# Optimization experiments

Measured on AMD Instinct MI355X. Metric: run time of the kernel, lower is better.

## Reference

```python
import jax, jax.numpy as jnp
import numpy as np

K_BITS = 4
V_BITS = 4
GROUP_SIZE = 64
EPS = 1e-8


def _quant_dequant_per_token(x, bits):
    # TurboQuantProd: symmetric per-token (per head_dim vector) absmax quantization.
    qmax = 2.0 ** (bits - 1) - 1.0
    scale = jnp.maximum(jnp.max(jnp.abs(x), axis=-1, keepdims=True) / qmax, EPS)
    return jnp.clip(jnp.round(x / scale), -qmax, qmax) * scale


def _quant_dequant_grouped(x, bits, group_size):
    # TurboQuantValue: symmetric grouped absmax quantization along head_dim.
    shp = x.shape
    xg = x.reshape(shp[:-1] + (shp[-1] // group_size, group_size))
    qmax = 2.0 ** (bits - 1) - 1.0
    scale = jnp.maximum(jnp.max(jnp.abs(xg), axis=-1, keepdims=True) / qmax, EPS)
    dq = jnp.clip(jnp.round(xg / scale), -qmax, qmax) * scale
    return dq.reshape(shp)


def setup_inputs() -> dict:
    key = jax.random.key(0)
    kq, kk, kv = jax.random.split(key, 3)
    B, H, S, D = 2, 16, 2048, 128
    query = jax.random.normal(kq, (B, H, S, D), dtype=jnp.float32)
    k = jax.random.normal(kk, (B, H, S, D), dtype=jnp.float32)
    v = jax.random.normal(kv, (B, H, S, D), dtype=jnp.float32)
    causal_mask = jnp.tril(jnp.ones((S, S), dtype=bool))[None, None]  # [1,1,S,S]
    return {"query": query, "key": k, "value": v, "causal_mask": causal_mask}


def reference(query, key, value, causal_mask):
    # Non-protected path: quantize K per-token, V grouped, then fused dequant + SDPA.
    head_dim = query.shape[-1]
    scale = 1.0 / np.sqrt(head_dim).astype(np.float32)
    dq_key = _quant_dequant_per_token(key, K_BITS)
    dq_value = _quant_dequant_grouped(value, V_BITS, GROUP_SIZE)
    scores = jnp.einsum('bhqd,bhkd->bhqk', query, dq_key) * scale
    scores = jnp.where(causal_mask, scores, -jnp.inf)
    weights = jax.nn.softmax(scores, axis=-1)
    output = jnp.einsum('bhqk,bhkd->bhqd', weights, dq_value)
    return (output, weights)
```

## Files before the change

kernel.cpp:

```cpp
#include <hip/hip_runtime.h>

#define SQ 2048
#define DD 128
#define BHN 32
#define SC2 0.12751741934f

typedef __attribute__((ext_vector_type(8))) short bf16x8;
typedef __attribute__((ext_vector_type(4))) float f32x4;

__device__ __forceinline__ unsigned short f2bf(float x){
  unsigned int u = __float_as_uint(x);
  unsigned int r = (u + 0x7FFFu + ((u >> 16) & 1u)) >> 16;
  return (unsigned short)r;
}
__device__ __forceinline__ unsigned pack2bf(float a, float b){
  return (unsigned)f2bf(a) | ((unsigned)f2bf(b) << 16);
}

__device__ __forceinline__ void gl_lds16(const void* g, void* l){
  __builtin_amdgcn_global_load_lds(
      (const __attribute__((address_space(1))) unsigned int*)g,
      (__attribute__((address_space(3))) unsigned int*)l, 16, 0, 0);
}

__global__ __launch_bounds__(256) void qd_kernel(const float* __restrict__ K,
                                                 const float* __restrict__ V,
                                                 char* __restrict__ dqK,
                                                 char* __restrict__ dqVt){
  __shared__ float Vlds[128*65];
  const int t = threadIdx.x;
  const int bh = blockIdx.x >> 5;
  const int stile = blockIdx.x & 31;
  const int tt = t >> 2;
  const int q4 = t & 3;
  const int s = stile*64 + tt;
  const long ebase = ((long)(bh*SQ + s))*DD + 32*q4;

  float vals[32];
  {
    const float4* kp = (const float4*)(K + ebase);
    float am = 0.f;
    #pragma unroll
    for (int j=0;j<8;j++){
      float4 v4 = kp[j];
      vals[4*j+0]=v4.x; vals[4*j+1]=v4.y; vals[4*j+2]=v4.z; vals[4*j+3]=v4.w;
      am = fmaxf(am, fmaxf(fmaxf(fabsf(v4.x),fabsf(v4.y)),fmaxf(fabsf(v4.z),fabsf(v4.w))));
    }
    am = fmaxf(am, __shfl_xor(am,1));
    am = fmaxf(am, __shfl_xor(am,2));
    const float sc = fmaxf(am/7.0f, 1e-8f);
    #pragma unroll
    for (int j=0;j<32;j++){
      float qv = rintf(vals[j]/sc);
      qv = fminf(7.f, fmaxf(-7.f, qv));
      vals[j] = qv*sc;
    }
    const long rowb = ((long)(bh*SQ + s))*256;
    const int swz = (s & 7) << 4;
    #pragma unroll
    for (int c=0;c<4;c++){
      uint4 w;
      w.x = pack2bf(vals[8*c+0], vals[8*c+1]);
      w.y = pack2bf(vals[8*c+2], vals[8*c+3]);
      w.z = pack2bf(vals[8*c+4], vals[8*c+5]);
      w.w = pack2bf(vals[8*c+6], vals[8*c+7]);
      *(uint4*)(dqK + rowb + ((64*q4 + 16*c) ^ swz)) = w;
    }
  }
  {
    const float4* vp = (const float4*)(V + ebase);
    float am = 0.f;
    #pragma unroll
    for (int j=0;j<8;j++){
      float4 v4 = vp[j];
      vals[4*j+0]=v4.x; vals[4*j+1]=v4.y; vals[4*j+2]=v4.z; vals[4*j+3]=v4.w;
      am = fmaxf(am, fmaxf(fmaxf(fabsf(v4.x),fabsf(v4.y)),fmaxf(fabsf(v4.z),fabsf(v4.w))));
    }
    am = fmaxf(am, __shfl_xor(am,1));
    const float sc = fmaxf(am/7.0f, 1e-8f);
    #pragma unroll
    for (int j=0;j<32;j++){
      float qv = rintf(vals[j]/sc);
      qv = fminf(7.f, fmaxf(-7.f, qv));
      Vlds[(32*q4 + j)*65 + tt] = qv*sc;
    }
  }
  __syncthreads();
  #pragma unroll
  for (int m=0;m<4;m++){
    const int chunk = m*256 + t;
    const int d = chunk >> 3;
    const int c = chunk & 7;
    uint4 w;
    const float* f = &Vlds[d*65 + 8*c];
    w.x = pack2bf(f[0], f[1]);
    w.y = pack2bf(f[2], f[3]);
    w.z = pack2bf(f[4], f[5]);
    w.w = pack2bf(f[6], f[7]);
    const long ob = ((long)(bh*DD + d))*4096 + (long)stile*128 + ((16*c) ^ ((d&7)<<4));
    *(uint4*)(dqVt + ob) = w;
  }
}

__global__ __launch_bounds__(512,2) void attn1_kernel(const float* __restrict__ Q,
    const char* __restrict__ dqK, const char* __restrict__ dqVt,
    float* __restrict__ Out, float* __restrict__ SinvG){
  __shared__ __attribute__((aligned(16))) char Kt[2][16384];
  __shared__ __attribute__((aligned(16))) char Vt[2][16384];
  __shared__ __attribute__((aligned(16))) char Et[8][4096];

  const int bid = blockIdx.x;
  const int xcd = bid & 7;
  const int loc = bid >> 3;
  const int bh  = xcd*4 + (loc & 3);
  const int p   = loc >> 2;
  const int t = threadIdx.x;
  const int lane = t & 63;
  const int w = t >> 6;
  const int s = w >> 2;
  const int ws = w & 3;
  const int l15 = lane & 15, l4 = lane >> 4;
  const int swz = (l15 & 7) << 4;

  const int qt   = s ? p : (15 - p);
  const int q0   = qt * 128;
  const int nktA = 2*(15 - p) + 2;
  const int nktB = 2*p + 2;
  const int myNkt = s ? nktB : nktA;
  const int rbase = q0 + 32*ws;

  bf16x8 qa[2][4];
  #pragma unroll
  for (int g=0; g<2; ++g){
    const float* qb = Q + ((long)(bh*SQ) + rbase + 16*g + l15)*DD + 8*l4;
    #pragma unroll
    for (int kk=0;kk<4;kk++){
      float4 a = *(const float4*)(qb + 32*kk);
      float4 b = *(const float4*)(qb + 32*kk + 4);
      bf16x8 r;
      r[0]=(short)f2bf(a.x); r[1]=(short)f2bf(a.y); r[2]=(short)f2bf(a.z); r[3]=(short)f2bf(a.w);
      r[4]=(short)f2bf(b.x); r[5]=(short)f2bf(b.y); r[6]=(short)f2bf(b.z); r[7]=(short)f2bf(b.w);
      qa[g][kk]=r;
    }
  }

  const char* Kb = dqK + (long)bh*SQ*256;
  const char* Vb = dqVt + (long)bh*DD*4096;

  const f32x4 z4 = {0.f,0.f,0.f,0.f};
  f32x4 oacc[2][8] = {{z4,z4,z4,z4,z4,z4,z4,z4},{z4,z4,z4,z4,z4,z4,z4,z4}};
  float ssum[2] = {0.f, 0.f};
  char* eb = &Et[w][0];

  auto stage = [&](int buf, int kt){
    const char* ks = Kb + (long)kt*16384;
    gl_lds16(ks + t*16,        &Kt[buf][t*16]);
    gl_lds16(ks + 8192 + t*16, &Kt[buf][8192 + t*16]);
    const char* vs = Vb + (long)kt*128;
    gl_lds16(vs + (long)(t>>3)*4096      + (t&7)*16, &Vt[buf][t*16]);
    gl_lds16(vs + (long)(64+(t>>3))*4096 + (t&7)*16, &Vt[buf][8192 + t*16]);
  };

  stage(0, 0);
  __syncthreads();
  int cur = 0;
  for (int kt=0; kt<nktA; ++kt){
    if (kt+1 < nktA) stage(cur^1, kt+1);

    if (kt < myNkt){
      f32x4 sacc[2][4] = {{z4,z4,z4,z4},{z4,z4,z4,z4}};
      {
        const char* kbase = &Kt[cur][0] + l15*256;
        __builtin_amdgcn_s_setprio(1);
        #pragma unroll
        for (int cf=0;cf<4;cf++){
          #pragma unroll
          for (int kk=0;kk<4;kk++){
            bf16x8 kb = *(const bf16x8*)(kbase + cf*4096 + ((64*kk+16*l4) ^ swz));
            sacc[0][cf] = __builtin_amdgcn_mfma_f32_16x16x32_bf16(kb, qa[0][kk], sacc[0][cf], 0,0,0);
            sacc[1][cf] = __builtin_amdgcn_mfma_f32_16x16x32_bf16(kb, qa[1][kk], sacc[1][cf], 0,0,0);
          }
        }
        __builtin_amdgcn_s_setprio(0);
      }

      const int k0 = kt*64;
      if (kt < 2*qt){
        #pragma unroll
        for (int g=0; g<2; ++g){
          const int lr = 16*g + l15;
          #pragma unroll
          for (int cf=0;cf<4;cf++){
            float e0 = exp2f(sacc[g][cf][0]*SC2);
            float e1 = exp2f(sacc[g][cf][1]*SC2);
            float e2 = exp2f(sacc[g][cf][2]*SC2);
            float e3 = exp2f(sacc[g][cf][3]*SC2);
            ssum[g] += (e0+e1) + (e2+e3);
            uint2 wp; wp.x = pack2bf(e0,e1); wp.y = pack2bf(e2,e3);
            *(uint2*)(eb + lr*128 + ((32*cf + 8*l4) ^ swz)) = wp;
          }
        }
      } else {
        #pragma unroll
        for (int g=0; g<2; ++g){
          const int lr = 16*g + l15;
          const int qrow = rbase + lr;
          #pragma unroll
          for (int cf=0;cf<4;cf++){
            const int tok0 = k0 + 16*cf + 4*l4;
            float e0 = (tok0+0 <= qrow) ? exp2f(sacc[g][cf][0]*SC2) : 0.f;
            float e1 = (tok0+1 <= qrow) ? exp2f(sacc[g][cf][1]*SC2) : 0.f;
            float e2 = (tok0+2 <= qrow) ? exp2f(sacc[g][cf][2]*SC2) : 0.f;
            float e3 = (tok0+3 <= qrow) ? exp2f(sacc[g][cf][3]*SC2) : 0.f;
            ssum[g] += (e0+e1) + (e2+e3);
            uint2 wp; wp.x = pack2bf(e0,e1); wp.y = pack2bf(e2,e3);
            *(uint2*)(eb + lr*128 + ((32*cf + 8*l4) ^ swz)) = wp;
          }
        }
      }

      {
        const char* vbase = &Vt[cur][0] + l15*128;
        __builtin_amdgcn_s_setprio(1);
        #pragma unroll
        for (int kc=0;kc<2;kc++){
          const int eo = (64*kc + 16*l4) ^ swz;
          bf16x8 ea0 = *(const bf16x8*)(eb + l15*128 + eo);
          bf16x8 ea1 = *(const bf16x8*)(eb + (16+l15)*128 + eo);
          #pragma unroll
          for (int df=0;df<8;df++){
            bf16x8 vv = *(const bf16x8*)(vbase + df*2048 + eo);
            oacc[0][df] = __builtin_amdgcn_mfma_f32_16x16x32_bf16(ea0, vv, oacc[0][df], 0,0,0);
            oacc[1][df] = __builtin_amdgcn_mfma_f32_16x16x32_bf16(ea1, vv, oacc[1][df], 0,0,0);
          }
        }
        __builtin_amdgcn_s_setprio(0);
      }
    }
    __syncthreads();
    cur ^= 1;
  }

  #pragma unroll
  for (int g=0; g<2; ++g){
    float sm = ssum[g];
    sm += __shfl_xor(sm, 16);
    sm += __shfl_xor(sm, 32);
    const float sinv = 1.0f / sm;
    if (l4 == 0) SinvG[(long)bh*SQ + rbase + 16*g + l15] = sinv;
    float invr[4];
    #pragma unroll
    for (int i=0;i<4;i++) invr[i] = __shfl(sinv, 4*l4+i);
    float* ob = Out + ((long)(bh*SQ) + rbase + 16*g)*DD;
    #pragma unroll
    for (int df=0;df<8;df++){
      #pragma unroll
      for (int i=0;i<4;i++)
        ob[(4*l4+i)*DD + 16*df + l15] = oacc[g][df][i]*invr[i];
    }
  }
}

__global__ __launch_bounds__(256) void attn2_kernel(const float* __restrict__ Q,
    const char* __restrict__ dqK, const float* __restrict__ SinvG,
    float* __restrict__ Wout){
  __shared__ __attribute__((aligned(16))) char Kt[2][16384];

  const int bid = blockIdx.x;
  const int xcd = bid & 7;
  const int loc = bid >> 3;
  const int bh  = xcd*4 + (loc >> 5);
  const int qt  = loc & 31;
  const int q0  = qt * 64;
  const int t = threadIdx.x;
  const int lane = t & 63;
  const int w = t >> 6;
  const int l15 = lane & 15, l4 = lane >> 4;
  const int swz = (l15 & 7) << 4;
  const int qrow = q0 + 16*w + l15;

  bf16x8 qa[4];
  {
    const float* qb = Q + ((long)(bh*SQ) + qrow)*DD + 8*l4;
    #pragma unroll
    for (int kk=0;kk<4;kk++){
      float4 a = *(const float4*)(qb + 32*kk);
      float4 b = *(const float4*)(qb + 32*kk + 4);
      bf16x8 r;
      r[0]=(short)f2bf(a.x); r[1]=(short)f2bf(a.y); r[2]=(short)f2bf(a.z); r[3]=(short)f2bf(a.w);
      r[4]=(short)f2bf(b.x); r[5]=(short)f2bf(b.y); r[6]=(short)f2bf(b.z); r[7]=(short)f2bf(b.w);
      qa[kk]=r;
    }
  }
  const float si = SinvG[(long)bh*SQ + qrow];
  const char* Kb = dqK + (long)bh*SQ*256;
  const int nkt = qt + 1;
  float* Wbase = Wout + (long)bh*SQ*SQ;
  float* wrow  = Wbase + (long)qrow*SQ;

  auto stage = [&](int buf, int kt){
    const char* ks = Kb + (long)kt*16384;
    #pragma unroll
    for (int i=0;i<4;i++)
      gl_lds16(ks + i*4096 + t*16, &Kt[buf][i*4096 + t*16]);
  };

  stage(0,0);
  __syncthreads();
  int cur = 0;
  const f32x4 z4 = {0.f,0.f,0.f,0.f};
  for (int kt=0; kt<nkt; ++kt){
    if (kt+1 < nkt) stage(cur^1, kt+1);
    const int k0 = kt*64;

    f32x4 sacc[4] = {z4,z4,z4,z4};
    {
      const char* kbase = &Kt[cur][0] + l15*256;
      __builtin_amdgcn_s_setprio(1);
      #pragma unroll
      for (int cf=0;cf<4;cf++){
        #pragma unroll
        for (int kk=0;kk<4;kk++){
          bf16x8 kb = *(const bf16x8*)(kbase + cf*4096 + ((64*kk+16*l4) ^ swz));
          sacc[cf] = __builtin_amdgcn_mfma_f32_16x16x32_bf16(kb, qa[kk], sacc[cf], 0,0,0);
        }
      }
      __builtin_amdgcn_s_setprio(0);
    }

    if (kt < qt){
      #pragma unroll
      for (int cf=0;cf<4;cf++){
        const int tok0 = k0 + 16*cf + 4*l4;
        float4 wv;
        wv.x = exp2f(sacc[cf][0]*SC2)*si;
        wv.y = exp2f(sacc[cf][1]*SC2)*si;
        wv.z = exp2f(sacc[cf][2]*SC2)*si;
        wv.w = exp2f(sacc[cf][3]*SC2)*si;
        *(float4*)(wrow + tok0) = wv;
      }
    } else {
      #pragma unroll
      for (int cf=0;cf<4;cf++){
        const int tok0 = k0 + 16*cf + 4*l4;
        float4 wv;
        wv.x = (tok0+0 <= qrow) ? exp2f(sacc[cf][0]*SC2)*si : 0.f;
        wv.y = (tok0+1 <= qrow) ? exp2f(sacc[cf][1]*SC2)*si : 0.f;
        wv.z = (tok0+2 <= qrow) ? exp2f(sacc[cf][2]*SC2)*si : 0.f;
        wv.w = (tok0+3 <= qrow) ? exp2f(sacc[cf][3]*SC2)*si : 0.f;
        *(float4*)(wrow + tok0) = wv;
      }
    }
    __syncthreads();
    cur ^= 1;
  }

  const int z0 = nkt*64;
  if (z0 < SQ){
    float* wr = Wbase + (long)(q0 + 16*w)*SQ;
    const float4 zz = {0.f,0.f,0.f,0.f};
    for (int r=0;r<16;r++){
      float* row = wr + (long)r*SQ;
      for (int c = z0 + 4*lane; c < SQ; c += 256)
        *(float4*)(row + c) = zz;
    }
  }
}

extern "C" void kernel_launch(void* const* d_in, const int* in_sizes, int n_in,
                              void* d_out, int out_size, void* d_ws, size_t ws_size,
                              hipStream_t stream) {
  const float* Q = (const float*)d_in[0];
  const float* K = (const float*)d_in[1];
  const float* V = (const float*)d_in[2];
  float* Out = (float*)d_out;
  float* Wout = (float*)d_out + (size_t)BHN*SQ*DD;
  char* dqK  = (char*)d_ws;
  char* dqVt = (char*)d_ws + (size_t)BHN*SQ*DD*2;
  float* SinvG = (float*)((char*)d_ws + (size_t)BHN*SQ*DD*4);

  qd_kernel<<<BHN*32, 256, 0, stream>>>(K, V, dqK, dqVt);
  attn1_kernel<<<256, 512, 0, stream>>>(Q, dqK, dqVt, Out, SinvG);
  attn2_kernel<<<1024, 256, 0, stream>>>(Q, dqK, SinvG, Wout);
}
```

Before: 280.9 us.

## Split attn1 into smaller 256-thread blocks and reorder attn2 block scheduling

attn1 now uses 256-thread blocks, each handling two 64-row query tiles paired as (31-p, p) for causal load balance, instead of 512-thread blocks over 128-row tiles. The grid doubles to 512, staging loops are widened so 256 threads fill the K/V tiles, and the per-wave E scratch shrinks. attn2's block index mapping now puts the query tile in the high bits and spreads heads across XCDs, so blocks with similar causal work run together. The aim is finer-grained load balance and more resident blocks, at the cost of more K/V tile reloads per query row.

```diff
diff --git a/kernel.cpp b/kernel.cpp
--- a/kernel.cpp
+++ b/kernel.cpp
@@ -102,12 +102,12 @@
   }
 }
 
-__global__ __launch_bounds__(512,2) void attn1_kernel(const float* __restrict__ Q,
+__global__ __launch_bounds__(256,2) void attn1_kernel(const float* __restrict__ Q,
     const char* __restrict__ dqK, const char* __restrict__ dqVt,
     float* __restrict__ Out, float* __restrict__ SinvG){
   __shared__ __attribute__((aligned(16))) char Kt[2][16384];
   __shared__ __attribute__((aligned(16))) char Vt[2][16384];
-  __shared__ __attribute__((aligned(16))) char Et[8][4096];
+  __shared__ __attribute__((aligned(16))) char Et[4][4096];
 
   const int bid = blockIdx.x;
   const int xcd = bid & 7;
@@ -117,16 +117,15 @@
   const int t = threadIdx.x;
   const int lane = t & 63;
   const int w = t >> 6;
-  const int s = w >> 2;
-  const int ws = w & 3;
+  const int s = w >> 1;
+  const int ws = w & 1;
   const int l15 = lane & 15, l4 = lane >> 4;
   const int swz = (l15 & 7) << 4;
 
-  const int qt   = s ? p : (15 - p);
-  const int q0   = qt * 128;
-  const int nktA = 2*(15 - p) + 2;
-  const int nktB = 2*p + 2;
-  const int myNkt = s ? nktB : nktA;
+  const int qt   = s ? p : (31 - p);
+  const int q0   = qt * 64;
+  const int nktA = 32 - p;
+  const int myNkt = qt + 1;
   const int rbase = q0 + 32*ws;
 
   bf16x8 qa[2][4];
@@ -154,11 +153,13 @@
 
   auto stage = [&](int buf, int kt){
     const char* ks = Kb + (long)kt*16384;
-    gl_lds16(ks + t*16,        &Kt[buf][t*16]);
-    gl_lds16(ks + 8192 + t*16, &Kt[buf][8192 + t*16]);
+    #pragma unroll
+    for (int i=0;i<4;i++)
+      gl_lds16(ks + i*4096 + t*16, &Kt[buf][i*4096 + t*16]);
     const char* vs = Vb + (long)kt*128;
-    gl_lds16(vs + (long)(t>>3)*4096      + (t&7)*16, &Vt[buf][t*16]);
-    gl_lds16(vs + (long)(64+(t>>3))*4096 + (t&7)*16, &Vt[buf][8192 + t*16]);
+    #pragma unroll
+    for (int i=0;i<4;i++)
+      gl_lds16(vs + (long)(i*32 + (t>>3))*4096 + (t&7)*16, &Vt[buf][i*4096 + t*16]);
   };
 
   stage(0, 0);
@@ -185,7 +186,7 @@
       }
 
       const int k0 = kt*64;
-      if (kt < 2*qt){
+      if (kt < qt){
         #pragma unroll
         for (int g=0; g<2; ++g){
           const int lr = 16*g + l15;
@@ -267,10 +268,9 @@
   __shared__ __attribute__((aligned(16))) char Kt[2][16384];
 
   const int bid = blockIdx.x;
-  const int xcd = bid & 7;
-  const int loc = bid >> 3;
-  const int bh  = xcd*4 + (loc >> 5);
-  const int qt  = loc & 31;
+  const int qt  = bid >> 5;
+  const int r   = bid & 31;
+  const int bh  = 4*(r & 7) + (r >> 3);
   const int q0  = qt * 64;
   const int t = threadIdx.x;
   const int lane = t & 63;
@@ -286,10 +286,10 @@
     for (int kk=0;kk<4;kk++){
       float4 a = *(const float4*)(qb + 32*kk);
       float4 b = *(const float4*)(qb + 32*kk + 4);
-      bf16x8 r;
-      r[0]=(short)f2bf(a.x); r[1]=(short)f2bf(a.y); r[2]=(short)f2bf(a.z); r[3]=(short)f2bf(a.w);
-      r[4]=(short)f2bf(b.x); r[5]=(short)f2bf(b.y); r[6]=(short)f2bf(b.z); r[7]=(short)f2bf(b.w);
-      qa[kk]=r;
+      bf16x8 r2;
+      r2[0]=(short)f2bf(a.x); r2[1]=(short)f2bf(a.y); r2[2]=(short)f2bf(a.z); r2[3]=(short)f2bf(a.w);
+      r2[4]=(short)f2bf(b.x); r2[5]=(short)f2bf(b.y); r2[6]=(short)f2bf(b.z); r2[7]=(short)f2bf(b.w);
+      qa[kk]=r2;
     }
   }
   const float si = SinvG[(long)bh*SQ + qrow];
@@ -359,8 +359,8 @@
   if (z0 < SQ){
     float* wr = Wbase + (long)(q0 + 16*w)*SQ;
     const float4 zz = {0.f,0.f,0.f,0.f};
-    for (int r=0;r<16;r++){
-      float* row = wr + (long)r*SQ;
+    for (int rr=0;rr<16;rr++){
+      float* row = wr + (long)rr*SQ;
       for (int c = z0 + 4*lane; c < SQ; c += 256)
         *(float4*)(row + c) = zz;
     }
@@ -380,6 +380,6 @@
   float* SinvG = (float*)((char*)d_ws + (size_t)BHN*SQ*DD*4);
 
   qd_kernel<<<BHN*32, 256, 0, stream>>>(K, V, dqK, dqVt);
-  attn1_kernel<<<256, 512, 0, stream>>>(Q, dqK, dqVt, Out, SinvG);
+  attn1_kernel<<<512, 256, 0, stream>>>(Q, dqK, dqVt, Out, SinvG);
   attn2_kernel<<<1024, 256, 0, stream>>>(Q, dqK, SinvG, Wout);
 }
```

Result: faster. 272.5 us (-3.0%).
